# Kernel optimization log

Measured on AMD Instinct MI355X. Metric: run time of the kernel, lower is better.

Reference implementation:

```python
import jax, jax.numpy as jnp
import numpy as np

NUM_POINTS = 16384
OVERSAMPLE = 3
IMPORTANCE_RATIO = 0.75


def point_sample(feat, coords):
    """grid_sample(bilinear, align_corners=False, zero padding) at [0,1]^2 coords.
    feat: (N, C, H, W); coords: (N, P, 2) with coords[...,0]=x (width), [...,1]=y.
    Returns (N, C, P)."""
    N, C, H, W = feat.shape
    # grid_sample with g = 2c-1, align_corners=False -> pixel = c*size - 0.5
    x = coords[..., 0] * W - 0.5
    y = coords[..., 1] * H - 0.5
    x0 = jnp.floor(x)
    y0 = jnp.floor(y)
    x1 = x0 + 1.0
    y1 = y0 + 1.0
    wx1 = x - x0
    wx0 = 1.0 - wx1
    wy1 = y - y0
    wy0 = 1.0 - wy1
    featf = feat.reshape(N, C, H * W)

    def gather(yi, xi):
        valid = (xi >= 0) & (xi <= W - 1) & (yi >= 0) & (yi <= H - 1)
        xic = jnp.clip(xi, 0, W - 1).astype(jnp.int32)
        yic = jnp.clip(yi, 0, H - 1).astype(jnp.int32)
        idx = yic * W + xic  # (N, P)
        v = jnp.take_along_axis(featf, idx[:, None, :], axis=2)  # (N, C, P)
        return v * valid[:, None, :].astype(feat.dtype)

    out = (gather(y0, x0) * (wy0 * wx0)[:, None, :]
           + gather(y0, x1) * (wy0 * wx1)[:, None, :]
           + gather(y1, x0) * (wy1 * wx0)[:, None, :]
           + gather(y1, x1) * (wy1 * wx1)[:, None, :])
    return out


def calculate_uncertainty(logits):
    """logits: (N, C, P) -> (N, P) uncertainty = top2 - top1 (<= 0)."""
    if logits.shape[1] == 1:
        return -jnp.abs(logits)[:, 0, :]
    top2 = jax.lax.top_k(jnp.moveaxis(logits, 1, -1), 2)[0]  # (N, P, 2)
    return top2[..., 1] - top2[..., 0]


def sample_point_coords(coarse_logits):
    """get_uncertain_point_coords_with_randomness (torch.no_grad branch)."""
    N = coarse_logits.shape[0]
    num_sampled = NUM_POINTS * OVERSAMPLE
    num_imp = int(IMPORTANCE_RATIO * NUM_POINTS)
    num_rand = NUM_POINTS - num_imp
    k1, k2 = jax.random.split(jax.random.key(7))
    cand = jax.random.uniform(k1, (N, num_sampled, 2), dtype=jnp.float32)
    cand_logits = point_sample(coarse_logits, cand)  # (N, C, S)
    unc = calculate_uncertainty(cand_logits)  # (N, S)
    idx = jax.lax.top_k(unc, num_imp)[1]  # (N, num_imp)
    imp = jnp.take_along_axis(cand, idx[..., None], axis=1)  # (N, num_imp, 2)
    rand = jax.random.uniform(k2, (N, num_rand, 2), dtype=jnp.float32)
    return jnp.concatenate([imp, rand], axis=1)  # (N, P, 2)


def point_head(fine, coarse_pts, w0, b0, w1, b1, w2, b2, wp, bp):
    x = jnp.concatenate([fine, coarse_pts], axis=1)  # (N, nin+C, P)
    for w, b in ((w0, b0), (w1, b1), (w2, b2)):
        x = jax.nn.relu(jnp.einsum('oc,ncp->nop', w, x) + b[None, :, None])
        x = jnp.concatenate([x, coarse_pts], axis=1)  # coarse_pred_each_layer
    return jnp.einsum('oc,ncp->nop', wp, x) + bp[None, :, None]  # (N, C, P)


def setup_inputs() -> dict:
    key = jax.random.key(0)
    ks = jax.random.split(key, 8)
    N, C, Hc, Wc = 8, 19, 64, 64
    nin, Hf, Wf = 256, 128, 128
    fin = nin + C  # 275
    return {
        'coarse_sem_seg_logits': jax.random.normal(ks[0], (N, C, Hc, Wc), jnp.float32),
        'features': jax.random.normal(ks[1], (N, nin, Hf, Wf), jnp.float32),
        'w0': jax.random.normal(ks[2], (nin, fin), jnp.float32) * (2.0 / fin) ** 0.5,
        'b0': jnp.zeros((nin,), jnp.float32),
        'w1': jax.random.normal(ks[3], (nin, fin), jnp.float32) * (2.0 / fin) ** 0.5,
        'b1': jnp.zeros((nin,), jnp.float32),
        'w2': jax.random.normal(ks[4], (nin, fin), jnp.float32) * (2.0 / fin) ** 0.5,
        'b2': jnp.zeros((nin,), jnp.float32),
        'wp': jax.random.normal(ks[5], (C, fin), jnp.float32) * 0.001,
        'bp': jnp.zeros((C,), jnp.float32),
    }


def reference(coarse_sem_seg_logits, features, w0, b0, w1, b1, w2, b2, wp, bp):
    # training-mode forward of PointRendSemSegHead
    point_coords = jax.lax.stop_gradient(
        sample_point_coords(jax.lax.stop_gradient(coarse_sem_seg_logits)))
    coarse_pts = point_sample(coarse_sem_seg_logits, point_coords)  # (N, C, P)
    fine_pts = point_sample(features, point_coords)  # (N, nin, P)
    point_logits = point_head(fine_pts, coarse_pts, w0, b0, w1, b1, w2, b2, wp, bp)
    return coarse_sem_seg_logits, point_logits, point_coords
```

## Files before the change

### kernel.cpp

```cpp
#include <hip/hip_runtime.h>
#include <stdint.h>

#pragma clang fp contract(off)

#define NB    8
#define CCH   19
#define CSTR  20
#define FCH   256
#define FIN   275
#define KP    288
#define NPTS  16384
#define NSAMP 49152
#define NIMP  12288
#define NRAND 4096
#define SORT_M 65536
#define CHUNK  8192
#define TP    128
#define XROW  640
#define WBF_OFF (4u << 20)
#define CTR_OFF (4718592u)
#define FTR_OFF (8u << 20)
#define FTR_BYTES (134217728ull / 2)

typedef __attribute__((ext_vector_type(8))) short bf16x8;
typedef __attribute__((ext_vector_type(4))) float f32x4;

__host__ __device__ __forceinline__ uint32_t rotl32(uint32_t v, int r) {
  return (v << r) | (v >> (32 - r));
}

__host__ __device__ __forceinline__ void tf2x32(uint32_t k0, uint32_t k1,
                                                uint32_t x0, uint32_t x1,
                                                uint32_t* o0, uint32_t* o1) {
  const uint32_t ks2 = k0 ^ k1 ^ 0x1BD11BDAu;
  x0 += k0; x1 += k1;
#define TF_R(r) { x0 += x1; x1 = rotl32(x1, (r)); x1 ^= x0; }
  TF_R(13) TF_R(15) TF_R(26) TF_R(6)
  x0 += k1;  x1 += ks2 + 1u;
  TF_R(17) TF_R(29) TF_R(16) TF_R(24)
  x0 += ks2; x1 += k0 + 2u;
  TF_R(13) TF_R(15) TF_R(26) TF_R(6)
  x0 += k0;  x1 += k1 + 3u;
  TF_R(17) TF_R(29) TF_R(16) TF_R(24)
  x0 += k1;  x1 += ks2 + 4u;
  TF_R(13) TF_R(15) TF_R(26) TF_R(6)
  x0 += ks2; x1 += k0 + 5u;
#undef TF_R
  *o0 = x0; *o1 = x1;
}

__device__ __forceinline__ float u01_at(uint32_t k0, uint32_t k1, uint32_t i) {
  uint32_t o0, o1;
  tf2x32(k0, k1, 0u, i, &o0, &o1);
  const uint32_t b = o0 ^ o1;
  const float f = __uint_as_float((b >> 9) | 0x3f800000u) - 1.0f;
  return fmaxf(0.0f, f);
}

__device__ __forceinline__ unsigned short f2bf(float f) {
  const uint32_t u = __float_as_uint(f);
  return (unsigned short)((u + 0x7fffu + ((u >> 16) & 1u)) >> 16);
}

__device__ __forceinline__ float bf2f(unsigned short h) {
  return __uint_as_float((uint32_t)h << 16);
}

template <int SZ>
__device__ __forceinline__ void interp(float cx, float cy, int* off, float* wgt) {
  const float X = cx * (float)SZ - 0.5f, Y = cy * (float)SZ - 0.5f;
  const float x0f = floorf(X), y0f = floorf(Y);
  const float fx = X - x0f, fy = Y - y0f;
  const float wx0 = 1.0f - fx, wy0 = 1.0f - fy;
  const int x0 = (int)x0f, y0 = (int)y0f;
  const int x0c = min(max(x0, 0), SZ - 1), x1c = min(max(x0 + 1, 0), SZ - 1);
  const int y0c = min(max(y0, 0), SZ - 1), y1c = min(max(y0 + 1, 0), SZ - 1);
  const bool vx0 = (x0 >= 0) & (x0 <= SZ - 1), vx1 = (x0 >= -1) & (x0 <= SZ - 2);
  const bool vy0 = (y0 >= 0) & (y0 <= SZ - 1), vy1 = (y0 >= -1) & (y0 <= SZ - 2);
  off[0] = y0c * SZ + x0c; wgt[0] = (vy0 & vx0) ? wy0 * wx0 : 0.0f;
  off[1] = y0c * SZ + x1c; wgt[1] = (vy0 & vx1) ? wy0 * fx  : 0.0f;
  off[2] = y1c * SZ + x0c; wgt[2] = (vy1 & vx0) ? fy  * wx0 : 0.0f;
  off[3] = y1c * SZ + x1c; wgt[3] = (vy1 & vx1) ? fy  * fx  : 0.0f;
}

__global__ __launch_bounds__(256) void ctr_transpose(
    const float* __restrict__ coarse, float* __restrict__ ctr) {
  __shared__ float tile[CCH][257];
  const int b = blockIdx.x;
  const int nn = b >> 4, px0 = (b & 15) * 256;
  const int t = threadIdx.x;
  const float* src = coarse + (size_t)nn * (CCH * 4096) + px0;
#pragma unroll
  for (int c = 0; c < CCH; ++c) tile[c][t] = src[c * 4096 + t];
  __syncthreads();
  float v[CSTR];
#pragma unroll
  for (int c = 0; c < CCH; ++c) v[c] = tile[c][t];
  v[19] = 0.0f;
  float* dst = ctr + ((size_t)(nn << 12) + px0 + t) * CSTR;
#pragma unroll
  for (int k = 0; k < 5; ++k) {
    f32x4 x; x[0] = v[4*k]; x[1] = v[4*k+1]; x[2] = v[4*k+2]; x[3] = v[4*k+3];
    *(f32x4*)(dst + 4 * k) = x;
  }
}

__global__ __launch_bounds__(256) void fusedA(
    const float* __restrict__ feats, unsigned short* __restrict__ ftr,
    const float* __restrict__ ctr, unsigned long long* __restrict__ keys,
    const float* __restrict__ w0, const float* __restrict__ w1,
    const float* __restrict__ w2, const float* __restrict__ wpw,
    unsigned short* __restrict__ wbf, unsigned short* __restrict__ wpb,
    uint32_t k1a, uint32_t k1b, int use_tr) {
  __shared__ unsigned short tile[64][66];
  const int bid = blockIdx.x;
  const int t = threadIdx.x;

  if (bid < 8192) {
    if (!use_tr) return;
    const int nn = bid >> 10;
    const int ct = (bid >> 8) & 3;
    const int pt = bid & 255;
    const int c0 = ct * 64, p0 = pt * 64;
    const float* src = feats + ((size_t)nn << 22);
#pragma unroll 4
    for (int k = 0; k < 16; ++k) {
      const int c = 4 * k + (t >> 6);
      const int p = t & 63;
      tile[p][c] = f2bf(src[((size_t)(c0 + c) << 14) + p0 + p]);
    }
    __syncthreads();
    const int p = t >> 2, q = t & 3;
    const int cb = q * 16;
    uint32_t w[8];
#pragma unroll
    for (int m = 0; m < 8; ++m)
      w[m] = (uint32_t)tile[p][cb + 2 * m] | ((uint32_t)tile[p][cb + 2 * m + 1] << 16);
    unsigned short* dst = ftr + ((((size_t)nn << 14) + p0 + p) << 8) + c0 + cb;
    *(uint4*)(dst)     = make_uint4(w[0], w[1], w[2], w[3]);
    *(uint4*)(dst + 8) = make_uint4(w[4], w[5], w[6], w[7]);
  } else if (bid < 10240) {
    const int tid = (bid - 8192) * 256 + t;
    const int nn = tid >> 16, s = tid & (SORT_M - 1);
    if (s >= NSAMP) { keys[tid] = 0xFFFFFFFFFFFFFFFFull; return; }
    const uint32_t ci = (uint32_t)(((unsigned)nn * NSAMP + (unsigned)s) * 2);
    const float cx = u01_at(k1a, k1b, ci);
    const float cy = u01_at(k1a, k1b, ci + 1);
    const float X = cx * 64.0f - 0.5f, Y = cy * 64.0f - 0.5f;
    const float x0f = floorf(X), y0f = floorf(Y);
    const float fx = X - x0f, fy = Y - y0f;
    const float wx0 = 1.0f - fx, wy0 = 1.0f - fy;
    const int x0 = (int)x0f, y0 = (int)y0f;
    const int x0c = min(max(x0, 0), 63), x1c = min(max(x0 + 1, 0), 63);
    const int y0c = min(max(y0, 0), 63), y1c = min(max(y0 + 1, 0), 63);
    const bool vx0 = (x0 >= 0) & (x0 <= 63), vx1 = (x0 >= -1) & (x0 <= 62);
    const bool vy0 = (y0 >= 0) & (y0 <= 63), vy1 = (y0 >= -1) & (y0 <= 62);
    const float w00 = (vy0 & vx0) ? wy0 * wx0 : 0.0f;
    const float w01 = (vy0 & vx1) ? wy0 * fx  : 0.0f;
    const float w10 = (vy1 & vx0) ? fy  * wx0 : 0.0f;
    const float w11 = (vy1 & vx1) ? fy  * fx  : 0.0f;
    const float* rb = ctr + ((size_t)nn << 12) * CSTR;
    const float* r0 = rb + (size_t)(y0c * 64 + x0c) * CSTR;
    const float* r1 = rb + (size_t)(y0c * 64 + x1c) * CSTR;
    const float* r2 = rb + (size_t)(y1c * 64 + x0c) * CSTR;
    const float* r3 = rb + (size_t)(y1c * 64 + x1c) * CSTR;
    float m1 = -3.402823466e38f, m2 = -3.402823466e38f;
#pragma unroll
    for (int k = 0; k < 5; ++k) {
      const f32x4 x0v = *(const f32x4*)(r0 + 4 * k);
      const f32x4 x1v = *(const f32x4*)(r1 + 4 * k);
      const f32x4 x2v = *(const f32x4*)(r2 + 4 * k);
      const f32x4 x3v = *(const f32x4*)(r3 + 4 * k);
#pragma unroll
      for (int e = 0; e < 4; ++e) {
        const int c = 4 * k + e;
        if (c < CCH) {
          const float v = ((x0v[e] * w00 + x1v[e] * w01) + x2v[e] * w10) + x3v[e] * w11;
          if (v > m1) { m2 = m1; m1 = v; } else if (v > m2) { m2 = v; }
        }
      }
    }
    const float unc = m2 - m1;
    const uint32_t b = __float_as_uint(unc);
    const uint32_t asc = (b & 0x80000000u) ? ~b : (b | 0x80000000u);
    keys[tid] = ((unsigned long long)(~asc) << 32) | (uint32_t)s;
  } else {
    const int i = (bid - 10240) * 256 + t;
    if (i < 3 * 256 * KP) {
      const int L = i / (256 * KP);
      const int rem = i - L * (256 * KP);
      const int o = rem / KP, k = rem - o * KP;
      const float* W = (L == 0) ? w0 : (L == 1) ? w1 : w2;
      wbf[i] = (k < FIN) ? f2bf(W[o * FIN + k]) : (unsigned short)0;
    } else {
      const int j = i - 3 * 256 * KP;
      const int o = j / KP, k = j - o * KP;
      wpb[j] = (o < CCH && k < FIN) ? f2bf(wpw[o * FIN + k]) : (unsigned short)0;
    }
  }
}

__global__ __launch_bounds__(1024) void bitonic_local(unsigned long long* __restrict__ keys) {
  __shared__ unsigned long long s[CHUNK];
  const int cb = blockIdx.x;
  unsigned long long* a = keys + (size_t)cb * CHUNK;
  const unsigned gbase = (unsigned)(cb * CHUNK) & (SORT_M - 1);
  for (int i = threadIdx.x; i < CHUNK; i += 1024) s[i] = a[i];
  __syncthreads();
  for (int k = 2; k <= CHUNK; k <<= 1) {
    for (int j = k >> 1; j > 0; j >>= 1) {
      for (int pid = threadIdx.x; pid < CHUNK / 2; pid += 1024) {
        const int i = ((pid & ~(j - 1)) << 1) | (pid & (j - 1));
        const int l = i | j;
        const bool up = (((gbase + i) & k) == 0);
        const unsigned long long x = s[i], y = s[l];
        if ((x > y) == up) { s[i] = y; s[l] = x; }
      }
      __syncthreads();
    }
  }
  for (int i = threadIdx.x; i < CHUNK; i += 1024) a[i] = s[i];
}

__global__ __launch_bounds__(256) void bitonic_global(unsigned long long* __restrict__ keys,
                                                      int k, int j, int ppb_shift) {
  const int t = blockIdx.x * blockDim.x + threadIdx.x;
  const int b = t >> ppb_shift, pid = t & ((1 << ppb_shift) - 1);
  const int i = ((pid & ~(j - 1)) << 1) | (pid & (j - 1));
  const int l = i | j;
  const bool up = ((i & k) == 0);
  unsigned long long* a = keys + ((size_t)b << 16);
  const unsigned long long x = a[i], y = a[l];
  if ((x > y) == up) { a[i] = y; a[l] = x; }
}

__global__ __launch_bounds__(1024) void bitonic_finish(unsigned long long* __restrict__ keys,
                                                       int k) {
  __shared__ unsigned long long s[CHUNK];
  const int cb = blockIdx.x;
  unsigned long long* a = keys + (size_t)cb * CHUNK;
  const unsigned gi0 = (unsigned)(cb * CHUNK) & (SORT_M - 1);
  for (int i = threadIdx.x; i < CHUNK; i += 1024) s[i] = a[i];
  __syncthreads();
  const bool up = ((gi0 & k) == 0);
  for (int j = CHUNK >> 1; j > 0; j >>= 1) {
    for (int pid = threadIdx.x; pid < CHUNK / 2; pid += 1024) {
      const int i = ((pid & ~(j - 1)) << 1) | (pid & (j - 1));
      const int l = i | j;
      const unsigned long long x = s[i], y = s[l];
      if ((x > y) == up) { s[i] = y; s[l] = x; }
    }
    __syncthreads();
  }
  for (int i = threadIdx.x; i < CHUNK; i += 1024) a[i] = s[i];
}

__global__ __launch_bounds__(1024) void finlow_coords(
    const unsigned long long* __restrict__ keys, float* __restrict__ outc,
    uint32_t k1a, uint32_t k1b, uint32_t k2a, uint32_t k2b) {
  __shared__ unsigned long long s[CHUNK];
  const int nn = blockIdx.x >> 1, half = blockIdx.x & 1;
  const unsigned long long* a = keys + ((size_t)nn << 16) + half * CHUNK;
  for (int i = threadIdx.x; i < CHUNK; i += 1024) s[i] = a[i];
  __syncthreads();
  for (int j = CHUNK >> 1; j > 0; j >>= 1) {
    for (int pid = threadIdx.x; pid < CHUNK / 2; pid += 1024) {
      const int i = ((pid & ~(j - 1)) << 1) | (pid & (j - 1));
      const int l = i | j;
      const unsigned long long x = s[i], y = s[l];
      if (x > y) { s[i] = y; s[l] = x; }
    }
    __syncthreads();
  }
  const int pb = half * CHUNK;
  for (int q = threadIdx.x; q < CHUNK; q += 1024) {
    const int p = pb + q;
    float cx, cy;
    if (p < NIMP) {
      const unsigned idx = (unsigned)(s[q] & 0xFFFFFFFFu);
      const uint32_t ci = ((unsigned)nn * NSAMP + idx) * 2;
      cx = u01_at(k1a, k1b, ci);
      cy = u01_at(k1a, k1b, ci + 1);
    } else {
      const uint32_t ri = ((unsigned)nn * NRAND + (unsigned)(p - NIMP)) * 2;
      cx = u01_at(k2a, k2b, ri);
      cy = u01_at(k2a, k2b, ri + 1);
    }
    float* o = outc + (((size_t)nn << 14) + p) * 2;
    o[0] = cx; o[1] = cy;
  }
}

template <int USE_TR>
__global__ __launch_bounds__(512, 2) void fused_mfma(
    const float* __restrict__ coarse, const float* __restrict__ feats,
    const unsigned short* __restrict__ ftr, const float* __restrict__ ctr,
    const float* __restrict__ b0, const float* __restrict__ b1,
    const float* __restrict__ b2, const float* __restrict__ bp,
    const unsigned short* __restrict__ wbf, const unsigned short* __restrict__ wpb,
    const float* __restrict__ pc, float* __restrict__ outl) {
  __shared__ __align__(16) unsigned short xp[TP * (XROW / 2)];

  const int t = threadIdx.x;
  const int nn = blockIdx.x >> 7;
  const int pbase = (blockIdx.x & 127) * TP;

  int offF[4]; float wgtF[4];
  int offC[4]; float wgtC[4];
  int offFc[4]; float wgtFc[4];
  {
    const float2 c = *(const float2*)(pc + ((size_t)nn * NPTS + pbase + (t >> 2)) * 2);
    interp<128>(c.x, c.y, offF, wgtF);
  }
  {
    const float2 c = *(const float2*)(pc + ((size_t)nn * NPTS + pbase + (t & 127)) * 2);
    interp<64>(c.x, c.y, offC, wgtC);
    if (!USE_TR) interp<128>(c.x, c.y, offFc, wgtFc);
  }

  if (USE_TR) {
    const int p = t >> 2, q = t & 3;
    const unsigned short* base = ftr + ((size_t)nn << 22) + q * 64;
    const unsigned short* n0 = base + ((size_t)offF[0] << 8);
    const unsigned short* n1 = base + ((size_t)offF[1] << 8);
    const unsigned short* n2 = base + ((size_t)offF[2] << 8);
    const unsigned short* n3 = base + ((size_t)offF[3] << 8);
    const float g0 = wgtF[0], g1 = wgtF[1], g2 = wgtF[2], g3 = wgtF[3];
    const unsigned swzp = (unsigned)(p & 7) << 4;
#pragma unroll
    for (int m = 0; m < 8; ++m) {
      const bf16x8 a = *(const bf16x8*)(n0 + m * 8);
      const bf16x8 bq = *(const bf16x8*)(n1 + m * 8);
      const bf16x8 c = *(const bf16x8*)(n2 + m * 8);
      const bf16x8 d = *(const bf16x8*)(n3 + m * 8);
      uint32_t u[4];
#pragma unroll
      for (int e = 0; e < 4; ++e) {
        float v0 = fmaf(bf2f((unsigned short)a[2 * e]), g0,
                   fmaf(bf2f((unsigned short)bq[2 * e]), g1,
                   fmaf(bf2f((unsigned short)c[2 * e]), g2,
                        bf2f((unsigned short)d[2 * e]) * g3)));
        float v1 = fmaf(bf2f((unsigned short)a[2 * e + 1]), g0,
                   fmaf(bf2f((unsigned short)bq[2 * e + 1]), g1,
                   fmaf(bf2f((unsigned short)c[2 * e + 1]), g2,
                        bf2f((unsigned short)d[2 * e + 1]) * g3)));
        u[e] = (uint32_t)f2bf(v0) | ((uint32_t)f2bf(v1) << 16);
      }
      *(uint4*)((char*)xp + p * XROW + (((unsigned)(q * 128 + m * 16)) ^ swzp)) =
          make_uint4(u[0], u[1], u[2], u[3]);
    }
    if (t < TP) {
      const int pp = t;
      const float* rb = ctr + ((size_t)nn << 12) * CSTR;
      const float* r0 = rb + (size_t)offC[0] * CSTR;
      const float* r1 = rb + (size_t)offC[1] * CSTR;
      const float* r2 = rb + (size_t)offC[2] * CSTR;
      const float* r3 = rb + (size_t)offC[3] * CSTR;
      const float h0 = wgtC[0], h1 = wgtC[1], h2 = wgtC[2], h3 = wgtC[3];
      unsigned short hs[32];
#pragma unroll
      for (int k = 0; k < 5; ++k) {
        const f32x4 x0v = *(const f32x4*)(r0 + 4 * k);
        const f32x4 x1v = *(const f32x4*)(r1 + 4 * k);
        const f32x4 x2v = *(const f32x4*)(r2 + 4 * k);
        const f32x4 x3v = *(const f32x4*)(r3 + 4 * k);
#pragma unroll
        for (int e = 0; e < 4; ++e) {
          const int c = 4 * k + e;
          if (c < CCH)
            hs[c] = f2bf(fmaf(x0v[e], h0, fmaf(x1v[e], h1,
                         fmaf(x2v[e], h2, x3v[e] * h3))));
        }
      }
#pragma unroll
      for (int c = CCH; c < 32; ++c) hs[c] = 0;
      const unsigned swzc = (unsigned)(pp & 7) << 4;
#pragma unroll
      for (int k = 0; k < 4; ++k) {
        uint4 u;
        u.x = (uint32_t)hs[8*k]   | ((uint32_t)hs[8*k+1] << 16);
        u.y = (uint32_t)hs[8*k+2] | ((uint32_t)hs[8*k+3] << 16);
        u.z = (uint32_t)hs[8*k+4] | ((uint32_t)hs[8*k+5] << 16);
        u.w = (uint32_t)hs[8*k+6] | ((uint32_t)hs[8*k+7] << 16);
        *(uint4*)((char*)xp + pp * XROW + (((unsigned)(512 + 16 * k)) ^ swzc)) = u;
      }
    }
  } else {
    for (int i = t; i < (KP / 2) * TP; i += 512) {
      const int p = i & (TP - 1);
      const int c0 = (i >> 7) * 2;
      float v0 = 0.0f, v1 = 0.0f;
      if (c0 < FCH) {
        const float* fb0 = feats + ((size_t)nn << 22) + ((size_t)c0 << 14);
        const float* fb1 = fb0 + 16384;
        v0 = ((fb0[offFc[0]] * wgtFc[0] + fb0[offFc[1]] * wgtFc[1])
             + fb0[offFc[2]] * wgtFc[2]) + fb0[offFc[3]] * wgtFc[3];
        v1 = ((fb1[offFc[0]] * wgtFc[0] + fb1[offFc[1]] * wgtFc[1])
             + fb1[offFc[2]] * wgtFc[2]) + fb1[offFc[3]] * wgtFc[3];
      } else if (c0 < FIN) {
        const float* cb0 = coarse + (size_t)nn * (CCH * 4096) + (size_t)(c0 - FCH) * 4096;
        v0 = ((cb0[offC[0]] * wgtC[0] + cb0[offC[1]] * wgtC[1])
             + cb0[offC[2]] * wgtC[2]) + cb0[offC[3]] * wgtC[3];
        if (c0 + 1 < FIN) {
          const float* cb1 = cb0 + 4096;
          v1 = ((cb1[offC[0]] * wgtC[0] + cb1[offC[1]] * wgtC[1])
               + cb1[offC[2]] * wgtC[2]) + cb1[offC[3]] * wgtC[3];
        }
      }
      const uint32_t u = (uint32_t)f2bf(v0) | ((uint32_t)f2bf(v1) << 16);
      *(uint32_t*)((char*)xp + p * XROW + (((unsigned)(c0 * 2)) ^ ((unsigned)(p & 7) << 4))) = u;
    }
  }

  const int lane = t & 63, wave = t >> 6;
  const int wm = wave & 3, wn = wave >> 2;
  const int l15 = lane & 15, g = lane >> 4;
  const unsigned swz = (unsigned)(l15 & 7) << 4;
  const char* xpB = (const char*)xp;

#pragma unroll
  for (int L = 0; L < 3; ++L) {
    __syncthreads();
    const float* Bv = (L == 0) ? b0 : (L == 1) ? b1 : b2;
    const unsigned short* wL = wbf + (size_t)L * (256 * KP);
    const unsigned short* wbase = wL + (size_t)(wm * 64 + l15) * KP + g * 8;

    f32x4 acc[4][4];
#pragma unroll
    for (int mt = 0; mt < 4; ++mt)
#pragma unroll
      for (int nt = 0; nt < 4; ++nt) acc[mt][nt] = (f32x4)(0.0f);

    for (int ks = 0; ks < 9; ++ks) {
      const bf16x8 a0 = *(const bf16x8*)(wbase + 0 * 16 * KP + ks * 32);
      const bf16x8 a1 = *(const bf16x8*)(wbase + 1 * 16 * KP + ks * 32);
      const bf16x8 a2 = *(const bf16x8*)(wbase + 2 * 16 * KP + ks * 32);
      const bf16x8 a3 = *(const bf16x8*)(wbase + 3 * 16 * KP + ks * 32);
      const unsigned kb = (unsigned)(ks * 64 + g * 16) ^ swz;
      const bf16x8 q0 = *(const bf16x8*)(xpB + (wn * 64 +  0 + l15) * XROW + kb);
      const bf16x8 q1 = *(const bf16x8*)(xpB + (wn * 64 + 16 + l15) * XROW + kb);
      const bf16x8 q2 = *(const bf16x8*)(xpB + (wn * 64 + 32 + l15) * XROW + kb);
      const bf16x8 q3 = *(const bf16x8*)(xpB + (wn * 64 + 48 + l15) * XROW + kb);
#pragma unroll
      for (int nt = 0; nt < 4; ++nt) {
        const bf16x8 bq = (nt == 0) ? q0 : (nt == 1) ? q1 : (nt == 2) ? q2 : q3;
        acc[0][nt] = __builtin_amdgcn_mfma_f32_16x16x32_bf16(a0, bq, acc[0][nt], 0, 0, 0);
        acc[1][nt] = __builtin_amdgcn_mfma_f32_16x16x32_bf16(a1, bq, acc[1][nt], 0, 0, 0);
        acc[2][nt] = __builtin_amdgcn_mfma_f32_16x16x32_bf16(a2, bq, acc[2][nt], 0, 0, 0);
        acc[3][nt] = __builtin_amdgcn_mfma_f32_16x16x32_bf16(a3, bq, acc[3][nt], 0, 0, 0);
      }
    }
    __syncthreads();

#pragma unroll
    for (int mt = 0; mt < 4; ++mt) {
      const int ch0 = wm * 64 + mt * 16 + (g << 2);
      const float4 bv = *(const float4*)(Bv + ch0);
#pragma unroll
      for (int nt = 0; nt < 4; ++nt) {
        const int p = wn * 64 + nt * 16 + l15;
        const f32x4 v = acc[mt][nt];
        const unsigned short h0 = f2bf(fmaxf(v[0] + bv.x, 0.0f));
        const unsigned short h1 = f2bf(fmaxf(v[1] + bv.y, 0.0f));
        const unsigned short h2 = f2bf(fmaxf(v[2] + bv.z, 0.0f));
        const unsigned short h3 = f2bf(fmaxf(v[3] + bv.w, 0.0f));
        uint2 u;
        u.x = (uint32_t)h0 | ((uint32_t)h1 << 16);
        u.y = (uint32_t)h2 | ((uint32_t)h3 << 16);
        *(uint2*)((char*)xp + p * XROW + (((unsigned)(ch0 * 2)) ^ swz)) = u;
      }
    }
  }
  __syncthreads();

  const unsigned short* hb0 = wpb + (size_t)l15 * KP + g * 8;
  const unsigned short* hb1 = wpb + (size_t)(16 + l15) * KP + g * 8;
  f32x4 hacc0 = (f32x4)(0.0f), hacc1 = (f32x4)(0.0f);
  for (int ks = 0; ks < 9; ++ks) {
    const unsigned kb = (unsigned)(ks * 64 + g * 16) ^ swz;
    const bf16x8 hbq = *(const bf16x8*)(xpB + (wave * 16 + l15) * XROW + kb);
    const bf16x8 ha0 = *(const bf16x8*)(hb0 + ks * 32);
    const bf16x8 ha1 = *(const bf16x8*)(hb1 + ks * 32);
    hacc0 = __builtin_amdgcn_mfma_f32_16x16x32_bf16(ha0, hbq, hacc0, 0, 0, 0);
    hacc1 = __builtin_amdgcn_mfma_f32_16x16x32_bf16(ha1, hbq, hacc1, 0, 0, 0);
  }
  const int p = pbase + wave * 16 + l15;
#pragma unroll
  for (int j = 0; j < 4; ++j) {
    const int ch0 = (g << 2) + j;
    outl[((size_t)nn * CCH + ch0) * NPTS + p] = hacc0[j] + bp[ch0];
    const int ch1 = 16 + (g << 2) + j;
    if (ch1 < CCH)
      outl[((size_t)nn * CCH + ch1) * NPTS + p] = hacc1[j] + bp[ch1];
  }
}

extern "C" void kernel_launch(void* const* d_in, const int* in_sizes, int n_in,
                              void* d_out, int out_size, void* d_ws, size_t ws_size,
                              hipStream_t stream) {
  const float* coarse = (const float*)d_in[0];
  const float* feats  = (const float*)d_in[1];
  const float* w0 = (const float*)d_in[2]; const float* b0 = (const float*)d_in[3];
  const float* w1 = (const float*)d_in[4]; const float* b1 = (const float*)d_in[5];
  const float* w2 = (const float*)d_in[6]; const float* b2 = (const float*)d_in[7];
  const float* wp = (const float*)d_in[8]; const float* bp = (const float*)d_in[9];

  float* out0 = (float*)d_out;
  float* outL = out0 + 622592;
  float* outC = outL + 2490368;

  unsigned long long* keys = (unsigned long long*)d_ws;
  unsigned short* wbf = (unsigned short*)((char*)d_ws + WBF_OFF);
  unsigned short* wpb = wbf + 3 * 256 * KP;
  float* ctr = (float*)((char*)d_ws + CTR_OFF);
  unsigned short* ftr = (unsigned short*)((char*)d_ws + FTR_OFF);
  const int use_tr = (ws_size >= (size_t)FTR_OFF + FTR_BYTES) ? 1 : 0;

  uint32_t k1a, k1b, k2a, k2b;
  tf2x32(0u, 7u, 0u, 0u, &k1a, &k1b);
  tf2x32(0u, 7u, 0u, 1u, &k2a, &k2b);

  hipMemcpyAsync(out0, coarse, 622592 * sizeof(float),
                 hipMemcpyDeviceToDevice, stream);

  ctr_transpose<<<128, 256, 0, stream>>>(coarse, ctr);

  fusedA<<<11140, 256, 0, stream>>>(feats, ftr, ctr, keys,
                                    w0, w1, w2, wp, wbf, wpb, k1a, k1b, use_tr);

  bitonic_local<<<64, 1024, 0, stream>>>(keys);
  bitonic_global<<<1024, 256, 0, stream>>>(keys, 16384, 8192, 15);
  bitonic_finish<<<64, 1024, 0, stream>>>(keys, 16384);
  bitonic_global<<<1024, 256, 0, stream>>>(keys, 32768, 16384, 15);
  bitonic_global<<<1024, 256, 0, stream>>>(keys, 32768, 8192, 15);
  bitonic_finish<<<64, 1024, 0, stream>>>(keys, 32768);
  bitonic_global<<<1024, 256, 0, stream>>>(keys, 65536, 32768, 15);
  bitonic_global<<<512, 256, 0, stream>>>(keys, 65536, 16384, 14);
  bitonic_global<<<256, 256, 0, stream>>>(keys, 65536, 8192, 13);
  finlow_coords<<<16, 1024, 0, stream>>>(keys, outC, k1a, k1b, k2a, k2b);

  if (use_tr)
    fused_mfma<1><<<1024, 512, 0, stream>>>(coarse, feats, ftr, ctr, b0, b1, b2,
                                            bp, wbf, wpb, outC, outL);
  else
    fused_mfma<0><<<1024, 512, 0, stream>>>(coarse, feats, ftr, ctr, b0, b1, b2,
                                            bp, wbf, wpb, outC, outL);
}
```

Baseline: 398.3 us.

## Halve point tile in fused MLP kernel, raise occupancy, prefetch weights, swizzle blocks

```diff
diff --git a/kernel.cpp b/kernel.cpp
--- a/kernel.cpp
+++ b/kernel.cpp
@@ -15,7 +15,7 @@
 #define NRAND 4096
 #define SORT_M 65536
 #define CHUNK  8192
-#define TP    128
+#define TP    64
 #define XROW  640
 #define WBF_OFF (4u << 20)
 #define CTR_OFF (4718592u)
@@ -292,7 +292,7 @@
 }
 
 template <int USE_TR>
-__global__ __launch_bounds__(512, 2) void fused_mfma(
+__global__ __launch_bounds__(512, 4) void fused_mfma(
     const float* __restrict__ coarse, const float* __restrict__ feats,
     const unsigned short* __restrict__ ftr, const float* __restrict__ ctr,
     const float* __restrict__ b0, const float* __restrict__ b1,
@@ -302,25 +302,26 @@
   __shared__ __align__(16) unsigned short xp[TP * (XROW / 2)];
 
   const int t = threadIdx.x;
-  const int nn = blockIdx.x >> 7;
-  const int pbase = (blockIdx.x & 127) * TP;
+  const int bid = ((int)blockIdx.x & 7) * 256 + ((int)blockIdx.x >> 3);
+  const int nn = bid >> 8;
+  const int pbase = (bid & 255) * TP;
 
   int offF[4]; float wgtF[4];
   int offC[4]; float wgtC[4];
   int offFc[4]; float wgtFc[4];
   {
-    const float2 c = *(const float2*)(pc + ((size_t)nn * NPTS + pbase + (t >> 2)) * 2);
+    const float2 c = *(const float2*)(pc + ((size_t)nn * NPTS + pbase + (t >> 3)) * 2);
     interp<128>(c.x, c.y, offF, wgtF);
   }
   {
-    const float2 c = *(const float2*)(pc + ((size_t)nn * NPTS + pbase + (t & 127)) * 2);
+    const float2 c = *(const float2*)(pc + ((size_t)nn * NPTS + pbase + (t & 63)) * 2);
     interp<64>(c.x, c.y, offC, wgtC);
     if (!USE_TR) interp<128>(c.x, c.y, offFc, wgtFc);
   }
 
   if (USE_TR) {
-    const int p = t >> 2, q = t & 3;
-    const unsigned short* base = ftr + ((size_t)nn << 22) + q * 64;
+    const int p = t >> 3, q = t & 7;
+    const unsigned short* base = ftr + ((size_t)nn << 22) + q * 32;
     const unsigned short* n0 = base + ((size_t)offF[0] << 8);
     const unsigned short* n1 = base + ((size_t)offF[1] << 8);
     const unsigned short* n2 = base + ((size_t)offF[2] << 8);
@@ -328,7 +329,7 @@
     const float g0 = wgtF[0], g1 = wgtF[1], g2 = wgtF[2], g3 = wgtF[3];
     const unsigned swzp = (unsigned)(p & 7) << 4;
 #pragma unroll
-    for (int m = 0; m < 8; ++m) {
+    for (int m = 0; m < 4; ++m) {
       const bf16x8 a = *(const bf16x8*)(n0 + m * 8);
       const bf16x8 bq = *(const bf16x8*)(n1 + m * 8);
       const bf16x8 c = *(const bf16x8*)(n2 + m * 8);
@@ -346,7 +347,7 @@
                         bf2f((unsigned short)d[2 * e + 1]) * g3)));
         u[e] = (uint32_t)f2bf(v0) | ((uint32_t)f2bf(v1) << 16);
       }
-      *(uint4*)((char*)xp + p * XROW + (((unsigned)(q * 128 + m * 16)) ^ swzp)) =
+      *(uint4*)((char*)xp + p * XROW + (((unsigned)((q * 32 + m * 8) * 2)) ^ swzp)) =
           make_uint4(u[0], u[1], u[2], u[3]);
     }
     if (t < TP) {
@@ -388,7 +389,7 @@
   } else {
     for (int i = t; i < (KP / 2) * TP; i += 512) {
       const int p = i & (TP - 1);
-      const int c0 = (i >> 7) * 2;
+      const int c0 = (i >> 6) * 2;
       float v0 = 0.0f, v1 = 0.0f;
       if (c0 < FCH) {
         const float* fb0 = feats + ((size_t)nn << 22) + ((size_t)c0 << 14);
@@ -425,30 +426,35 @@
     const unsigned short* wL = wbf + (size_t)L * (256 * KP);
     const unsigned short* wbase = wL + (size_t)(wm * 64 + l15) * KP + g * 8;
 
-    f32x4 acc[4][4];
+    f32x4 acc[4][2];
 #pragma unroll
     for (int mt = 0; mt < 4; ++mt)
 #pragma unroll
-      for (int nt = 0; nt < 4; ++nt) acc[mt][nt] = (f32x4)(0.0f);
-
+      for (int nt = 0; nt < 2; ++nt) acc[mt][nt] = (f32x4)(0.0f);
+
+    bf16x8 a0 = *(const bf16x8*)(wbase + 0 * 16 * KP);
+    bf16x8 a1 = *(const bf16x8*)(wbase + 1 * 16 * KP);
+    bf16x8 a2 = *(const bf16x8*)(wbase + 2 * 16 * KP);
+    bf16x8 a3 = *(const bf16x8*)(wbase + 3 * 16 * KP);
     for (int ks = 0; ks < 9; ++ks) {
-      const bf16x8 a0 = *(const bf16x8*)(wbase + 0 * 16 * KP + ks * 32);
-      const bf16x8 a1 = *(const bf16x8*)(wbase + 1 * 16 * KP + ks * 32);
-      const bf16x8 a2 = *(const bf16x8*)(wbase + 2 * 16 * KP + ks * 32);
-      const bf16x8 a3 = *(const bf16x8*)(wbase + 3 * 16 * KP + ks * 32);
+      const bf16x8 c0v = a0, c1v = a1, c2v = a2, c3v = a3;
+      if (ks < 8) {
+        a0 = *(const bf16x8*)(wbase + 0 * 16 * KP + (ks + 1) * 32);
+        a1 = *(const bf16x8*)(wbase + 1 * 16 * KP + (ks + 1) * 32);
+        a2 = *(const bf16x8*)(wbase + 2 * 16 * KP + (ks + 1) * 32);
+        a3 = *(const bf16x8*)(wbase + 3 * 16 * KP + (ks + 1) * 32);
+      }
       const unsigned kb = (unsigned)(ks * 64 + g * 16) ^ swz;
-      const bf16x8 q0 = *(const bf16x8*)(xpB + (wn * 64 +  0 + l15) * XROW + kb);
-      const bf16x8 q1 = *(const bf16x8*)(xpB + (wn * 64 + 16 + l15) * XROW + kb);
-      const bf16x8 q2 = *(const bf16x8*)(xpB + (wn * 64 + 32 + l15) * XROW + kb);
-      const bf16x8 q3 = *(const bf16x8*)(xpB + (wn * 64 + 48 + l15) * XROW + kb);
-#pragma unroll
-      for (int nt = 0; nt < 4; ++nt) {
-        const bf16x8 bq = (nt == 0) ? q0 : (nt == 1) ? q1 : (nt == 2) ? q2 : q3;
-        acc[0][nt] = __builtin_amdgcn_mfma_f32_16x16x32_bf16(a0, bq, acc[0][nt], 0, 0, 0);
-        acc[1][nt] = __builtin_amdgcn_mfma_f32_16x16x32_bf16(a1, bq, acc[1][nt], 0, 0, 0);
-        acc[2][nt] = __builtin_amdgcn_mfma_f32_16x16x32_bf16(a2, bq, acc[2][nt], 0, 0, 0);
-        acc[3][nt] = __builtin_amdgcn_mfma_f32_16x16x32_bf16(a3, bq, acc[3][nt], 0, 0, 0);
-      }
+      const bf16x8 q0 = *(const bf16x8*)(xpB + (wn * 32 + 0 + l15) * XROW + kb);
+      const bf16x8 q1 = *(const bf16x8*)(xpB + (wn * 32 + 16 + l15) * XROW + kb);
+      acc[0][0] = __builtin_amdgcn_mfma_f32_16x16x32_bf16(c0v, q0, acc[0][0], 0, 0, 0);
+      acc[1][0] = __builtin_amdgcn_mfma_f32_16x16x32_bf16(c1v, q0, acc[1][0], 0, 0, 0);
+      acc[2][0] = __builtin_amdgcn_mfma_f32_16x16x32_bf16(c2v, q0, acc[2][0], 0, 0, 0);
+      acc[3][0] = __builtin_amdgcn_mfma_f32_16x16x32_bf16(c3v, q0, acc[3][0], 0, 0, 0);
+      acc[0][1] = __builtin_amdgcn_mfma_f32_16x16x32_bf16(c0v, q1, acc[0][1], 0, 0, 0);
+      acc[1][1] = __builtin_amdgcn_mfma_f32_16x16x32_bf16(c1v, q1, acc[1][1], 0, 0, 0);
+      acc[2][1] = __builtin_amdgcn_mfma_f32_16x16x32_bf16(c2v, q1, acc[2][1], 0, 0, 0);
+      acc[3][1] = __builtin_amdgcn_mfma_f32_16x16x32_bf16(c3v, q1, acc[3][1], 0, 0, 0);
     }
     __syncthreads();
 
@@ -457,8 +463,8 @@
       const int ch0 = wm * 64 + mt * 16 + (g << 2);
       const float4 bv = *(const float4*)(Bv + ch0);
 #pragma unroll
-      for (int nt = 0; nt < 4; ++nt) {
-        const int p = wn * 64 + nt * 16 + l15;
+      for (int nt = 0; nt < 2; ++nt) {
+        const int p = wn * 32 + nt * 16 + l15;
         const f32x4 v = acc[mt][nt];
         const unsigned short h0 = f2bf(fmaxf(v[0] + bv.x, 0.0f));
         const unsigned short h1 = f2bf(fmaxf(v[1] + bv.y, 0.0f));
@@ -473,25 +479,21 @@
   }
   __syncthreads();
 
-  const unsigned short* hb0 = wpb + (size_t)l15 * KP + g * 8;
-  const unsigned short* hb1 = wpb + (size_t)(16 + l15) * KP + g * 8;
-  f32x4 hacc0 = (f32x4)(0.0f), hacc1 = (f32x4)(0.0f);
+  const int hmt = wave >> 2, hnt = wave & 3;
+  const unsigned short* hbase = wpb + (size_t)(hmt * 16 + l15) * KP + g * 8;
+  f32x4 hacc = (f32x4)(0.0f);
   for (int ks = 0; ks < 9; ++ks) {
     const unsigned kb = (unsigned)(ks * 64 + g * 16) ^ swz;
-    const bf16x8 hbq = *(const bf16x8*)(xpB + (wave * 16 + l15) * XROW + kb);
-    const bf16x8 ha0 = *(const bf16x8*)(hb0 + ks * 32);
-    const bf16x8 ha1 = *(const bf16x8*)(hb1 + ks * 32);
-    hacc0 = __builtin_amdgcn_mfma_f32_16x16x32_bf16(ha0, hbq, hacc0, 0, 0, 0);
-    hacc1 = __builtin_amdgcn_mfma_f32_16x16x32_bf16(ha1, hbq, hacc1, 0, 0, 0);
-  }
-  const int p = pbase + wave * 16 + l15;
+    const bf16x8 ha = *(const bf16x8*)(hbase + ks * 32);
+    const bf16x8 hb = *(const bf16x8*)(xpB + (hnt * 16 + l15) * XROW + kb);
+    hacc = __builtin_amdgcn_mfma_f32_16x16x32_bf16(ha, hb, hacc, 0, 0, 0);
+  }
+  const int p = pbase + hnt * 16 + l15;
 #pragma unroll
   for (int j = 0; j < 4; ++j) {
-    const int ch0 = (g << 2) + j;
-    outl[((size_t)nn * CCH + ch0) * NPTS + p] = hacc0[j] + bp[ch0];
-    const int ch1 = 16 + (g << 2) + j;
-    if (ch1 < CCH)
-      outl[((size_t)nn * CCH + ch1) * NPTS + p] = hacc1[j] + bp[ch1];
+    const int ch = hmt * 16 + (g << 2) + j;
+    if (ch < CCH)
+      outl[((size_t)nn * CCH + ch) * NPTS + p] = hacc[j] + bp[ch];
   }
 }
 
@@ -540,9 +542,9 @@
   finlow_coords<<<16, 1024, 0, stream>>>(keys, outC, k1a, k1b, k2a, k2b);
 
   if (use_tr)
-    fused_mfma<1><<<1024, 512, 0, stream>>>(coarse, feats, ftr, ctr, b0, b1, b2,
+    fused_mfma<1><<<2048, 512, 0, stream>>>(coarse, feats, ftr, ctr, b0, b1, b2,
                                             bp, wbf, wpb, outC, outL);
   else
-    fused_mfma<0><<<1024, 512, 0, stream>>>(coarse, feats, ftr, ctr, b0, b1, b2,
+    fused_mfma<0><<<2048, 512, 0, stream>>>(coarse, feats, ftr, ctr, b0, b1, b2,
                                             bp, wbf, wpb, outC, outL);
 }
```

After: 367.2 us. 1.08x faster.
